# Kernel tuning notes

Hardware: AMD Instinct MI355X
Metric: run time of the kernel (lower is better)

The kernel has to match this reference:

```python
import jax, jax.numpy as jnp
import numpy as np

B, T, D = 4, 4096, 1024

def setup_inputs() -> dict:
    key = jax.random.key(0)
    ks = jax.random.split(key, 6)
    x = jax.random.normal(ks[0], (B, T, D), dtype=jnp.float32)
    mask = jax.random.randint(ks[1], (B, T), 0, 2).astype(bool)
    # torch nn.Linear init scale ~ 1/sqrt(fan_in); exact init unimportant for correctness baseline
    s = 1.0 / np.sqrt(D)
    W_qkv = jax.random.normal(ks[2], (3 * D, D), dtype=jnp.float32) * s
    b_qkv = jax.random.normal(ks[3], (3 * D,), dtype=jnp.float32) * s
    W_out = jax.random.normal(ks[4], (D, D), dtype=jnp.float32) * s
    b_out = jax.random.normal(ks[5], (D,), dtype=jnp.float32) * s
    return {"x": x, "mask": mask, "W_qkv": W_qkv, "b_qkv": b_qkv, "W_out": W_out, "b_out": b_out}

def reference(x, mask, W_qkv, b_qkv, W_out, b_out):
    # qkv projection: (B,T,D) @ (D,3D) + (3D,)
    qkv = jnp.einsum('btd,ed->bte', x, W_qkv) + b_qkv
    q, k, v = jnp.split(qkv, 3, axis=-1)  # each (B,T,D)
    q = q / jnp.linalg.norm(q, axis=-1, keepdims=True)
    k = k / jnp.linalg.norm(k, axis=-1, keepdims=True)
    k = jnp.where(mask[..., None], 0.0, k)  # masked_fill(mask, 0)
    kv = jnp.sum(k * v, axis=-2, keepdims=True)  # (B,1,D) global feature sum
    out = kv * q  # (B,T,D)
    return jnp.einsum('btd,ed->bte', out, W_out) + b_out
```

## Files before the change

kernel.cpp:

```cpp
#include <hip/hip_runtime.h>
#include <stdint.h>


typedef short  short8   __attribute__((ext_vector_type(8)));
typedef float  floatx16 __attribute__((ext_vector_type(16)));

#define NT 32

__device__ __forceinline__ void async16(const void* g, void* l) {
  __builtin_amdgcn_global_load_lds((const __attribute__((address_space(1))) void*)g,
                                   (__attribute__((address_space(3))) void*)l, 16, 0, 0);
}

__device__ __forceinline__ uint16_t f2bf(float f) {
  union { float f; uint32_t u; } x; x.f = f;
  uint32_t u = x.u;
  return (uint16_t)((u + 0x7fffu + ((u >> 16) & 1u)) >> 16);
}
__device__ __forceinline__ float bf2f(uint16_t h) {
  union { uint32_t u; float f; } x; x.u = ((uint32_t)h) << 16; return x.f;
}
__device__ __forceinline__ uint32_t pack2(float a, float b) {
  return (uint32_t)f2bf(a) | ((uint32_t)f2bf(b) << 16);
}
__device__ __forceinline__ void upk8(uint4 u, float* f) {
  f[0]=bf2f((uint16_t)u.x); f[1]=bf2f((uint16_t)(u.x>>16));
  f[2]=bf2f((uint16_t)u.y); f[3]=bf2f((uint16_t)(u.y>>16));
  f[4]=bf2f((uint16_t)u.z); f[5]=bf2f((uint16_t)(u.z>>16));
  f[6]=bf2f((uint16_t)u.w); f[7]=bf2f((uint16_t)(u.w>>16));
}

__global__ __launch_bounds__(256) void cvt3(
    const float* __restrict__ a, uint16_t* __restrict__ ao, int na,
    const float* __restrict__ b, uint16_t* __restrict__ bo, int nb,
    const float* __restrict__ c, uint16_t* __restrict__ co, int nc) {
  int i = blockIdx.x * 256 + threadIdx.x;
  const float* in; uint16_t* out; int j = i;
  if (j < na) { in = a; out = ao; }
  else {
    j -= na;
    if (j < nb) { in = b; out = bo; }
    else { j -= nb; if (j >= nc) return; in = c; out = co; }
  }
  const float4* p = (const float4*)in;
  float4 u = p[(size_t)j * 2], v = p[(size_t)j * 2 + 1];
  uint4 o;
  o.x = pack2(u.x, u.y); o.y = pack2(u.z, u.w);
  o.z = pack2(v.x, v.y); o.w = pack2(v.z, v.w);
  ((uint4*)out)[j] = o;
}

#define MFMA_PHASE(Ac, Bc, kcv, STAGE, GATE) { \
    const int slot_ = (((kcv) ^ rsw) * 8); \
    const uint16_t* Ap_ = (Ac) + slot_; \
    const uint16_t* Bp_ = (Bc) + slot_; \
    short8 a0_ = *(const short8*)&Ap_[(wm * 128 +  0 + l31) * 32]; \
    short8 a1_ = *(const short8*)&Ap_[(wm * 128 + 32 + l31) * 32]; \
    short8 a2_ = *(const short8*)&Ap_[(wm * 128 + 64 + l31) * 32]; \
    short8 a3_ = *(const short8*)&Ap_[(wm * 128 + 96 + l31) * 32]; \
    short8 b0_ = *(const short8*)&Bp_[(wn * 64 +  0 + l31) * 32]; \
    short8 b1_ = *(const short8*)&Bp_[(wn * 64 + 32 + l31) * 32]; \
    STAGE; \
    __builtin_amdgcn_sched_barrier(0); \
    __builtin_amdgcn_s_barrier(); \
    asm volatile("s_waitcnt lgkmcnt(0)" ::: "memory"); \
    __builtin_amdgcn_s_setprio(1); \
    acc[0][0] = __builtin_amdgcn_mfma_f32_32x32x16_bf16(a0_, b0_, acc[0][0], 0, 0, 0); \
    acc[0][1] = __builtin_amdgcn_mfma_f32_32x32x16_bf16(a0_, b1_, acc[0][1], 0, 0, 0); \
    acc[1][0] = __builtin_amdgcn_mfma_f32_32x32x16_bf16(a1_, b0_, acc[1][0], 0, 0, 0); \
    acc[1][1] = __builtin_amdgcn_mfma_f32_32x32x16_bf16(a1_, b1_, acc[1][1], 0, 0, 0); \
    acc[2][0] = __builtin_amdgcn_mfma_f32_32x32x16_bf16(a2_, b0_, acc[2][0], 0, 0, 0); \
    acc[2][1] = __builtin_amdgcn_mfma_f32_32x32x16_bf16(a2_, b1_, acc[2][1], 0, 0, 0); \
    acc[3][0] = __builtin_amdgcn_mfma_f32_32x32x16_bf16(a3_, b0_, acc[3][0], 0, 0, 0); \
    acc[3][1] = __builtin_amdgcn_mfma_f32_32x32x16_bf16(a3_, b1_, acc[3][1], 0, 0, 0); \
    __builtin_amdgcn_s_setprio(0); \
    GATE; \
    __builtin_amdgcn_sched_barrier(0); \
    __builtin_amdgcn_s_barrier(); \
  }

__global__ __launch_bounds__(512, 2) void gemm1(
    const uint16_t* __restrict__ A, const uint16_t* __restrict__ Bw,
    const float* __restrict__ bias, uint16_t* __restrict__ Cb)
{
  __shared__ __align__(16) uint16_t As[4][8192];
  __shared__ __align__(16) uint16_t Bs[4][8192];
  const int tid = threadIdx.x;
  const int wave = tid >> 6, lane = tid & 63;
  const int l31 = lane & 31, khalf = lane >> 5;
  const int rsw = (l31 >> 1) & 3;
  const int wm = wave & 1, wn = wave >> 1;
  const int id = blockIdx.x;
  const int xcd = id & 7, w = id >> 3;
  const int tileM = ((w / 12) * 8 + xcd) * 256;
  const int tileN = (w % 12) * 256;

  const int srow = tid >> 2;
  const int sk   = (tid & 3) ^ ((tid >> 3) & 3);
  const uint16_t* gA = A  + (size_t)(tileM + srow) * 1024 + sk * 8;
  const uint16_t* gB = Bw + (size_t)(tileN + srow) * 1024 + sk * 8;

  floatx16 acc[4][2];
#pragma unroll
  for (int mi = 0; mi < 4; mi++)
#pragma unroll
    for (int ni = 0; ni < 2; ni++)
#pragma unroll
      for (int r = 0; r < 16; r++) acc[mi][ni][r] = 0.f;

#pragma unroll
  for (int t = 0; t < 3; ++t) {
    const size_t ko = (size_t)t * 32;
    async16(gA + ko,                      (char*)As[t] + wave * 1024);
    async16(gA + ko + (size_t)128 * 1024, (char*)As[t] + 8192 + wave * 1024);
    async16(gB + ko,                      (char*)Bs[t] + wave * 1024);
    async16(gB + ko + (size_t)128 * 1024, (char*)Bs[t] + 8192 + wave * 1024);
  }
  asm volatile("s_waitcnt vmcnt(8)" ::: "memory");
  __builtin_amdgcn_s_barrier();

#define STG_A1(tt) if ((tt) < NT) { const int c3_ = (tt) & 3; const size_t ko_ = (size_t)(tt) * 32; \
    async16(gA + ko_,                      (char*)As[c3_] + wave * 1024); \
    async16(gA + ko_ + (size_t)128 * 1024, (char*)As[c3_] + 8192 + wave * 1024); }
#define STG_B1(tt) if ((tt) < NT) { const int c3_ = (tt) & 3; const size_t ko_ = (size_t)(tt) * 32; \
    async16(gB + ko_,                      (char*)Bs[c3_] + wave * 1024); \
    async16(gB + ko_ + (size_t)128 * 1024, (char*)Bs[c3_] + 8192 + wave * 1024); }
#define GATE_ if (t + 3 < NT) { asm volatile("s_waitcnt vmcnt(8)" ::: "memory"); } \
    else if (t + 2 < NT) { asm volatile("s_waitcnt vmcnt(4)" ::: "memory"); } \
    else if (t + 1 < NT) { asm volatile("s_waitcnt vmcnt(0)" ::: "memory"); }

#pragma unroll 1
  for (int t = 0; t < NT; ++t) {
    const uint16_t* Ac = As[t & 3];
    const uint16_t* Bc = Bs[t & 3];
    MFMA_PHASE(Ac, Bc, khalf,     STG_A1(t + 3), )
    MFMA_PHASE(Ac, Bc, khalf + 2, STG_B1(t + 3), GATE_)
  }
#undef STG_A1
#undef STG_B1
#undef GATE_

#pragma unroll
  for (int mi = 0; mi < 4; mi++) {
    const int rbase = tileM + wm * 128 + mi * 32 + 4 * khalf;
#pragma unroll
    for (int ni = 0; ni < 2; ni++) {
      const int col = tileN + wn * 64 + ni * 32 + l31;
      const float bv = bias[col];
#pragma unroll
      for (int reg = 0; reg < 16; reg++) {
        const int row = rbase + (reg & 3) + 8 * (reg >> 2);
        Cb[(size_t)row * 3072 + col] = f2bf(acc[mi][ni][reg] + bv);
      }
    }
  }
}

__global__ __launch_bounds__(512, 2) void gemm2(
    const uint16_t* __restrict__ qkv, const float* __restrict__ invq,
    const uint16_t* __restrict__ Wp, const float* __restrict__ bias,
    float* __restrict__ Cf)
{
  __shared__ __align__(16) uint16_t As[4][8192];
  __shared__ __align__(16) uint16_t Bs[4][8192];
  const int tid = threadIdx.x;
  const int wave = tid >> 6, lane = tid & 63;
  const int l31 = lane & 31, khalf = lane >> 5;
  const int rsw = (l31 >> 1) & 3;
  const int wm = wave & 1, wn = wave >> 1;
  const int id = blockIdx.x;
  const int tileM = (id >> 2) * 256;
  const int tileN = (id & 3) * 256;
  const int batch = tileM >> 12;

  const int srow = tid >> 2;
  const int sk   = (tid & 3) ^ ((tid >> 3) & 3);
  const uint16_t* gA = qkv + (size_t)(tileM + srow) * 3072 + sk * 8;
  const uint16_t* gB = Wp + ((size_t)batch << 20) + (size_t)(tileN + srow) * 1024 + sk * 8;

  floatx16 acc[4][2];
#pragma unroll
  for (int mi = 0; mi < 4; mi++)
#pragma unroll
    for (int ni = 0; ni < 2; ni++)
#pragma unroll
      for (int r = 0; r < 16; r++) acc[mi][ni][r] = 0.f;

#pragma unroll
  for (int t = 0; t < 3; ++t) {
    const size_t ko = (size_t)t * 32;
    async16(gA + ko,                      (char*)As[t] + wave * 1024);
    async16(gA + ko + (size_t)128 * 3072, (char*)As[t] + 8192 + wave * 1024);
    async16(gB + ko,                      (char*)Bs[t] + wave * 1024);
    async16(gB + ko + (size_t)128 * 1024, (char*)Bs[t] + 8192 + wave * 1024);
  }
  asm volatile("s_waitcnt vmcnt(8)" ::: "memory");
  __builtin_amdgcn_s_barrier();

#define STG_A2(tt) if ((tt) < NT) { const int c3_ = (tt) & 3; const size_t ko_ = (size_t)(tt) * 32; \
    async16(gA + ko_,                      (char*)As[c3_] + wave * 1024); \
    async16(gA + ko_ + (size_t)128 * 3072, (char*)As[c3_] + 8192 + wave * 1024); }
#define STG_B2(tt) if ((tt) < NT) { const int c3_ = (tt) & 3; const size_t ko_ = (size_t)(tt) * 32; \
    async16(gB + ko_,                      (char*)Bs[c3_] + wave * 1024); \
    async16(gB + ko_ + (size_t)128 * 1024, (char*)Bs[c3_] + 8192 + wave * 1024); }
#define GATE_ if (t + 3 < NT) { asm volatile("s_waitcnt vmcnt(8)" ::: "memory"); } \
    else if (t + 2 < NT) { asm volatile("s_waitcnt vmcnt(4)" ::: "memory"); } \
    else if (t + 1 < NT) { asm volatile("s_waitcnt vmcnt(0)" ::: "memory"); }

#pragma unroll 1
  for (int t = 0; t < NT; ++t) {
    const uint16_t* Ac = As[t & 3];
    const uint16_t* Bc = Bs[t & 3];
    MFMA_PHASE(Ac, Bc, khalf,     STG_A2(t + 3), )
    MFMA_PHASE(Ac, Bc, khalf + 2, STG_B2(t + 3), GATE_)
  }
#undef STG_A2
#undef STG_B2
#undef GATE_

#pragma unroll
  for (int mi = 0; mi < 4; mi++) {
    const int rbase = tileM + wm * 128 + mi * 32 + 4 * khalf;
#pragma unroll
    for (int ni = 0; ni < 2; ni++) {
      const int col = tileN + wn * 64 + ni * 32 + l31;
      const float bv = bias[col];
#pragma unroll
      for (int reg = 0; reg < 16; reg++) {
        const int row = rbase + (reg & 3) + 8 * (reg >> 2);
        Cf[(size_t)row * 1024 + col] = fmaf(invq[row], acc[mi][ni][reg], bv);
      }
    }
  }
}

__global__ __launch_bounds__(256) void scale_w(
    const uint16_t* __restrict__ wo, const float* __restrict__ kv,
    uint16_t* __restrict__ wp)
{
  int i = blockIdx.x * 256 + threadIdx.x;
  int e = i << 3;
  int b = e >> 20;
  int k = e & 1023;
  uint4 w = *(const uint4*)(wo + (e & 0xFFFFF));
  float4 k0v = *(const float4*)(kv + (b << 10) + k);
  float4 k1v = *(const float4*)(kv + (b << 10) + k + 4);
  float wf[8]; upk8(w, wf);
  uint4 o;
  o.x = pack2(wf[0] * k0v.x, wf[1] * k0v.y);
  o.y = pack2(wf[2] * k0v.z, wf[3] * k0v.w);
  o.z = pack2(wf[4] * k1v.x, wf[5] * k1v.y);
  o.w = pack2(wf[6] * k1v.z, wf[7] * k1v.w);
  *(uint4*)(wp + e) = o;
}

__global__ __launch_bounds__(256) void detect_mask(const unsigned char* __restrict__ m,
                                                   int* __restrict__ flag) {
  int i = blockIdx.x * blockDim.x + threadIdx.x;
  int v = ((i & 3) != 0) ? (int)m[i] : 0;
  unsigned long long b = __ballot(v != 0);
  if ((threadIdx.x & 63) == 0 && b) atomicOr(flag, 1);
}

__global__ __launch_bounds__(256) void rownorm_kv(
    const uint16_t* __restrict__ qkv, const void* __restrict__ maskbuf,
    const int* __restrict__ flag, float* __restrict__ invq, float* __restrict__ kv)
{
  __shared__ float kvloc[1024];
  const int tid = threadIdx.x;
  for (int i = tid; i < 1024; i += 256) kvloc[i] = 0.f;
  __syncthreads();
  const int wave = tid >> 6, lane = tid & 63;
  const int b = blockIdx.x >> 7;
  const int chunk = blockIdx.x & 127;
  const int isU8 = *flag;
  const unsigned char* m8 = (const unsigned char*)maskbuf;
  const int* m32 = (const int*)maskbuf;

  float kvacc[16];
#pragma unroll
  for (int i = 0; i < 16; i++) kvacc[i] = 0.f;

  const int r0 = b * 4096 + chunk * 32 + wave * 8;
#pragma unroll 2
  for (int j = 0; j < 8; j++) {
    int r = r0 + j;
    const uint16_t* rp = qkv + (size_t)r * 3072;
    uint4 q0 = *(const uint4*)(rp + lane * 16);
    uint4 q1 = *(const uint4*)(rp + lane * 16 + 8);
    uint4 k0 = *(const uint4*)(rp + 1024 + lane * 16);
    uint4 k1 = *(const uint4*)(rp + 1024 + lane * 16 + 8);
    uint4 v0 = *(const uint4*)(rp + 2048 + lane * 16);
    uint4 v1 = *(const uint4*)(rp + 2048 + lane * 16 + 8);
    float qf[16], kf[16], vf[16];
    upk8(q0, qf); upk8(q1, qf + 8);
    upk8(k0, kf); upk8(k1, kf + 8);
    upk8(v0, vf); upk8(v1, vf + 8);
    float sq = 0.f, sk = 0.f;
#pragma unroll
    for (int i = 0; i < 16; i++) { sq = fmaf(qf[i], qf[i], sq); sk = fmaf(kf[i], kf[i], sk); }
    for (int off = 32; off; off >>= 1) { sq += __shfl_xor(sq, off); sk += __shfl_xor(sk, off); }
    float rq = rsqrtf(sq), rk = rsqrtf(sk);
    if (lane == 0) invq[r] = rq;
    int masked = isU8 ? (int)m8[r] : m32[r];
    if (!masked) {
#pragma unroll
      for (int i = 0; i < 16; i++) kvacc[i] = fmaf(kf[i] * rk, vf[i], kvacc[i]);
    }
  }
#pragma unroll
  for (int i = 0; i < 16; i++) atomicAdd(&kvloc[lane * 16 + i], kvacc[i]);
  __syncthreads();
  for (int i = tid; i < 1024; i += 256) atomicAdd(&kv[b * 1024 + i], kvloc[i]);
}

extern "C" void kernel_launch(void* const* d_in, const int* in_sizes, int n_in,
                              void* d_out, int out_size, void* d_ws, size_t ws_size,
                              hipStream_t stream) {
  const float* x     = (const float*)d_in[0];
  const void*  mask  = d_in[1];
  const float* W_qkv = (const float*)d_in[2];
  const float* b_qkv = (const float*)d_in[3];
  const float* W_out = (const float*)d_in[4];
  const float* b_out = (const float*)d_in[5];
  float* out = (float*)d_out;

  const int BT = 4 * 4096;
  const int D  = 1024;

  char* ws = (char*)d_ws;
  size_t off = 0;
  auto alloc = [&](size_t bytes) { size_t r = off; off += (bytes + 255) & ~(size_t)255; return r; };
  size_t o_xb   = alloc((size_t)BT * D * 2);
  size_t o_qkvb = alloc((size_t)BT * 3 * D * 2);
  size_t o_wq   = alloc((size_t)3 * D * D * 2);
  size_t o_wo   = alloc((size_t)D * D * 2);
  size_t o_wp   = alloc((size_t)4 * D * D * 2);
  size_t o_kv   = alloc((size_t)4 * D * 4 + 256);
  size_t o_invq = alloc((size_t)BT * 4);

  uint16_t* xb   = (uint16_t*)(ws + o_xb);
  uint16_t* qkvb = (uint16_t*)(ws + o_qkvb);
  uint16_t* wq   = (uint16_t*)(ws + o_wq);
  uint16_t* wo   = (uint16_t*)(ws + o_wo);
  uint16_t* wp   = (uint16_t*)(ws + o_wp);
  float*    kv   = (float*)(ws + o_kv);
  int*      flag = (int*)(ws + o_kv + (size_t)4 * D * 4);
  float*    invq = (float*)(ws + o_invq);

  hipMemsetAsync(ws + o_kv, 0, (size_t)4 * D * 4 + 256, stream);
  {
    int na = BT * D / 8, nb = 3 * D * D / 8, nc = D * D / 8;
    int tot = na + nb + nc;
    cvt3<<<dim3((tot + 255) / 256), 256, 0, stream>>>(x, xb, na, W_qkv, wq, nb, W_out, wo, nc);
  }
  detect_mask<<<dim3(64), 256, 0, stream>>>((const unsigned char*)mask, flag);
  gemm1<<<dim3(768), 512, 0, stream>>>(xb, wq, b_qkv, qkvb);
  rownorm_kv<<<dim3(512), 256, 0, stream>>>(qkvb, mask, flag, invq, kv);
  scale_w<<<dim3(4 * D * D / 8 / 256), 256, 0, stream>>>(wo, kv, wp);
  gemm2<<<dim3(256), 512, 0, stream>>>(qkvb, invq, wp, b_out, out);
}
```

Measured before the change: 334.9 us.

## Double-buffer LDS fragments in GEMM K-loop and remap gemm2 blocks across XCDs

Restructures both GEMM main loops so LDS fragment reads for the next K-half are issued before the MFMAs on the current fragments. This cuts the per-iteration barriers from two to one and overlaps LDS latency with matrix math. It also permutes gemm2 block indices so consecutive tiles sharing A rows land on the same XCD for better L2 reuse. The cost is more registers held for the fragment double buffer, which could hurt occupancy under launch_bounds(512,2).

Result: no change. 338.7 us (+1.1%).

```diff
diff --git a/kernel.cpp b/kernel.cpp
--- a/kernel.cpp
+++ b/kernel.cpp
@@ -50,33 +50,54 @@
   ((uint4*)out)[j] = o;
 }
 
-#define MFMA_PHASE(Ac, Bc, kcv, STAGE, GATE) { \
-    const int slot_ = (((kcv) ^ rsw) * 8); \
-    const uint16_t* Ap_ = (Ac) + slot_; \
-    const uint16_t* Bp_ = (Bc) + slot_; \
-    short8 a0_ = *(const short8*)&Ap_[(wm * 128 +  0 + l31) * 32]; \
-    short8 a1_ = *(const short8*)&Ap_[(wm * 128 + 32 + l31) * 32]; \
-    short8 a2_ = *(const short8*)&Ap_[(wm * 128 + 64 + l31) * 32]; \
-    short8 a3_ = *(const short8*)&Ap_[(wm * 128 + 96 + l31) * 32]; \
-    short8 b0_ = *(const short8*)&Bp_[(wn * 64 +  0 + l31) * 32]; \
-    short8 b1_ = *(const short8*)&Bp_[(wn * 64 + 32 + l31) * 32]; \
-    STAGE; \
+#define LOADF(kci, Ac, Bc, kcv) { \
+    const int sl_ = (((kcv) ^ rsw) * 8); \
+    const uint16_t* Ap_ = (Ac) + sl_; \
+    const uint16_t* Bp_ = (Bc) + sl_; \
+    fA[kci][0] = *(const short8*)&Ap_[(wm * 128 +  0 + l31) * 32]; \
+    fA[kci][1] = *(const short8*)&Ap_[(wm * 128 + 32 + l31) * 32]; \
+    fA[kci][2] = *(const short8*)&Ap_[(wm * 128 + 64 + l31) * 32]; \
+    fA[kci][3] = *(const short8*)&Ap_[(wm * 128 + 96 + l31) * 32]; \
+    fB[kci][0] = *(const short8*)&Bp_[(wn * 64 +  0 + l31) * 32]; \
+    fB[kci][1] = *(const short8*)&Bp_[(wn * 64 + 32 + l31) * 32]; }
+
+#define MFMA8(kci) { \
+    __builtin_amdgcn_s_setprio(1); \
+    acc[0][0] = __builtin_amdgcn_mfma_f32_32x32x16_bf16(fA[kci][0], fB[kci][0], acc[0][0], 0, 0, 0); \
+    acc[0][1] = __builtin_amdgcn_mfma_f32_32x32x16_bf16(fA[kci][0], fB[kci][1], acc[0][1], 0, 0, 0); \
+    acc[1][0] = __builtin_amdgcn_mfma_f32_32x32x16_bf16(fA[kci][1], fB[kci][0], acc[1][0], 0, 0, 0); \
+    acc[1][1] = __builtin_amdgcn_mfma_f32_32x32x16_bf16(fA[kci][1], fB[kci][1], acc[1][1], 0, 0, 0); \
+    acc[2][0] = __builtin_amdgcn_mfma_f32_32x32x16_bf16(fA[kci][2], fB[kci][0], acc[2][0], 0, 0, 0); \
+    acc[2][1] = __builtin_amdgcn_mfma_f32_32x32x16_bf16(fA[kci][2], fB[kci][1], acc[2][1], 0, 0, 0); \
+    acc[3][0] = __builtin_amdgcn_mfma_f32_32x32x16_bf16(fA[kci][3], fB[kci][0], acc[3][0], 0, 0, 0); \
+    acc[3][1] = __builtin_amdgcn_mfma_f32_32x32x16_bf16(fA[kci][3], fB[kci][1], acc[3][1], 0, 0, 0); \
+    __builtin_amdgcn_s_setprio(0); }
+
+#define GATE_(t) if ((t) + 3 < NT) { asm volatile("s_waitcnt vmcnt(8)" ::: "memory"); } \
+    else if ((t) + 2 < NT) { asm volatile("s_waitcnt vmcnt(4)" ::: "memory"); } \
+    else if ((t) + 1 < NT) { asm volatile("s_waitcnt vmcnt(0)" ::: "memory"); }
+
+#define KLOOP(STAGE) \
+  asm volatile("s_waitcnt vmcnt(8)" ::: "memory"); \
+  __builtin_amdgcn_s_barrier(); \
+  LOADF(0, As[0], Bs[0], khalf); \
+  _Pragma("unroll 1") \
+  for (int t = 0; t < NT; ++t) { \
+    STAGE(t + 3); \
+    const uint16_t* Ac_ = As[t & 3]; \
+    const uint16_t* Bc_ = Bs[t & 3]; \
+    LOADF(1, Ac_, Bc_, khalf + 2);       \
+    MFMA8(0);                            \
+    GATE_(t); \
+    asm volatile("s_waitcnt lgkmcnt(0)" ::: "memory"); \
     __builtin_amdgcn_sched_barrier(0); \
     __builtin_amdgcn_s_barrier(); \
-    asm volatile("s_waitcnt lgkmcnt(0)" ::: "memory"); \
-    __builtin_amdgcn_s_setprio(1); \
-    acc[0][0] = __builtin_amdgcn_mfma_f32_32x32x16_bf16(a0_, b0_, acc[0][0], 0, 0, 0); \
-    acc[0][1] = __builtin_amdgcn_mfma_f32_32x32x16_bf16(a0_, b1_, acc[0][1], 0, 0, 0); \
-    acc[1][0] = __builtin_amdgcn_mfma_f32_32x32x16_bf16(a1_, b0_, acc[1][0], 0, 0, 0); \
-    acc[1][1] = __builtin_amdgcn_mfma_f32_32x32x16_bf16(a1_, b1_, acc[1][1], 0, 0, 0); \
-    acc[2][0] = __builtin_amdgcn_mfma_f32_32x32x16_bf16(a2_, b0_, acc[2][0], 0, 0, 0); \
-    acc[2][1] = __builtin_amdgcn_mfma_f32_32x32x16_bf16(a2_, b1_, acc[2][1], 0, 0, 0); \
-    acc[3][0] = __builtin_amdgcn_mfma_f32_32x32x16_bf16(a3_, b0_, acc[3][0], 0, 0, 0); \
-    acc[3][1] = __builtin_amdgcn_mfma_f32_32x32x16_bf16(a3_, b1_, acc[3][1], 0, 0, 0); \
-    __builtin_amdgcn_s_setprio(0); \
-    GATE; \
-    __builtin_amdgcn_sched_barrier(0); \
-    __builtin_amdgcn_s_barrier(); \
+    if (t + 1 < NT) { \
+      const uint16_t* An_ = As[(t + 1) & 3]; \
+      const uint16_t* Bn_ = Bs[(t + 1) & 3]; \
+      LOADF(0, An_, Bn_, khalf);         \
+    } \
+    MFMA8(1);                            \
   }
 
 __global__ __launch_bounds__(512, 2) void gemm1(
@@ -108,37 +129,17 @@
 #pragma unroll
       for (int r = 0; r < 16; r++) acc[mi][ni][r] = 0.f;
 
-#pragma unroll
-  for (int t = 0; t < 3; ++t) {
-    const size_t ko = (size_t)t * 32;
-    async16(gA + ko,                      (char*)As[t] + wave * 1024);
-    async16(gA + ko + (size_t)128 * 1024, (char*)As[t] + 8192 + wave * 1024);
-    async16(gB + ko,                      (char*)Bs[t] + wave * 1024);
-    async16(gB + ko + (size_t)128 * 1024, (char*)Bs[t] + 8192 + wave * 1024);
-  }
-  asm volatile("s_waitcnt vmcnt(8)" ::: "memory");
-  __builtin_amdgcn_s_barrier();
-
-#define STG_A1(tt) if ((tt) < NT) { const int c3_ = (tt) & 3; const size_t ko_ = (size_t)(tt) * 32; \
+  short8 fA[2][4], fB[2][2];
+
+#define STG1(tt) if ((tt) < NT) { const int c3_ = (tt) & 3; const size_t ko_ = (size_t)(tt) * 32; \
     async16(gA + ko_,                      (char*)As[c3_] + wave * 1024); \
-    async16(gA + ko_ + (size_t)128 * 1024, (char*)As[c3_] + 8192 + wave * 1024); }
-#define STG_B1(tt) if ((tt) < NT) { const int c3_ = (tt) & 3; const size_t ko_ = (size_t)(tt) * 32; \
+    async16(gA + ko_ + (size_t)128 * 1024, (char*)As[c3_] + 8192 + wave * 1024); \
     async16(gB + ko_,                      (char*)Bs[c3_] + wave * 1024); \
     async16(gB + ko_ + (size_t)128 * 1024, (char*)Bs[c3_] + 8192 + wave * 1024); }
-#define GATE_ if (t + 3 < NT) { asm volatile("s_waitcnt vmcnt(8)" ::: "memory"); } \
-    else if (t + 2 < NT) { asm volatile("s_waitcnt vmcnt(4)" ::: "memory"); } \
-    else if (t + 1 < NT) { asm volatile("s_waitcnt vmcnt(0)" ::: "memory"); }
-
-#pragma unroll 1
-  for (int t = 0; t < NT; ++t) {
-    const uint16_t* Ac = As[t & 3];
-    const uint16_t* Bc = Bs[t & 3];
-    MFMA_PHASE(Ac, Bc, khalf,     STG_A1(t + 3), )
-    MFMA_PHASE(Ac, Bc, khalf + 2, STG_B1(t + 3), GATE_)
-  }
-#undef STG_A1
-#undef STG_B1
-#undef GATE_
+
+  STG1(0); STG1(1); STG1(2);
+  KLOOP(STG1)
+#undef STG1
 
 #pragma unroll
   for (int mi = 0; mi < 4; mi++) {
@@ -168,7 +169,7 @@
   const int l31 = lane & 31, khalf = lane >> 5;
   const int rsw = (l31 >> 1) & 3;
   const int wm = wave & 1, wn = wave >> 1;
-  const int id = blockIdx.x;
+  const int id = (blockIdx.x & 7) * 32 + (blockIdx.x >> 3);
   const int tileM = (id >> 2) * 256;
   const int tileN = (id & 3) * 256;
   const int batch = tileM >> 12;
@@ -186,37 +187,17 @@
 #pragma unroll
       for (int r = 0; r < 16; r++) acc[mi][ni][r] = 0.f;
 
-#pragma unroll
-  for (int t = 0; t < 3; ++t) {
-    const size_t ko = (size_t)t * 32;
-    async16(gA + ko,                      (char*)As[t] + wave * 1024);
-    async16(gA + ko + (size_t)128 * 3072, (char*)As[t] + 8192 + wave * 1024);
-    async16(gB + ko,                      (char*)Bs[t] + wave * 1024);
-    async16(gB + ko + (size_t)128 * 1024, (char*)Bs[t] + 8192 + wave * 1024);
-  }
-  asm volatile("s_waitcnt vmcnt(8)" ::: "memory");
-  __builtin_amdgcn_s_barrier();
-
-#define STG_A2(tt) if ((tt) < NT) { const int c3_ = (tt) & 3; const size_t ko_ = (size_t)(tt) * 32; \
+  short8 fA[2][4], fB[2][2];
+
+#define STG2(tt) if ((tt) < NT) { const int c3_ = (tt) & 3; const size_t ko_ = (size_t)(tt) * 32; \
     async16(gA + ko_,                      (char*)As[c3_] + wave * 1024); \
-    async16(gA + ko_ + (size_t)128 * 3072, (char*)As[c3_] + 8192 + wave * 1024); }
-#define STG_B2(tt) if ((tt) < NT) { const int c3_ = (tt) & 3; const size_t ko_ = (size_t)(tt) * 32; \
+    async16(gA + ko_ + (size_t)128 * 3072, (char*)As[c3_] + 8192 + wave * 1024); \
     async16(gB + ko_,                      (char*)Bs[c3_] + wave * 1024); \
     async16(gB + ko_ + (size_t)128 * 1024, (char*)Bs[c3_] + 8192 + wave * 1024); }
-#define GATE_ if (t + 3 < NT) { asm volatile("s_waitcnt vmcnt(8)" ::: "memory"); } \
-    else if (t + 2 < NT) { asm volatile("s_waitcnt vmcnt(4)" ::: "memory"); } \
-    else if (t + 1 < NT) { asm volatile("s_waitcnt vmcnt(0)" ::: "memory"); }
-
-#pragma unroll 1
-  for (int t = 0; t < NT; ++t) {
-    const uint16_t* Ac = As[t & 3];
-    const uint16_t* Bc = Bs[t & 3];
-    MFMA_PHASE(Ac, Bc, khalf,     STG_A2(t + 3), )
-    MFMA_PHASE(Ac, Bc, khalf + 2, STG_B2(t + 3), GATE_)
-  }
-#undef STG_A2
-#undef STG_B2
-#undef GATE_
+
+  STG2(0); STG2(1); STG2(2);
+  KLOOP(STG2)
+#undef STG2
 
 #pragma unroll
   for (int mi = 0; mi < 4; mi++) {
```
